# Kernel tuning notes

Hardware: AMD Instinct MI355X
Metric: run time of the kernel (lower is better)

Reference implementation:

```python
import jax, jax.numpy as jnp
import numpy as np

EPS = 1e-5


def setup_inputs() -> dict:
    key = jax.random.key(0)
    ks = jax.random.split(key, 6)
    B, N, F = 8, 8192, 64
    xyzs = jax.random.uniform(ks[0], (B, N, 3), dtype=jnp.float32)
    feats = jax.random.normal(ks[1], (B, N, F), dtype=jnp.float32)
    c_in = 3 + F  # 67
    dims = [(64, c_in), (64, 64), (128, 64)]
    inp = {"xyzs": xyzs, "feats": feats}
    for i, (co, ci) in enumerate(dims, start=1):
        inp[f"w{i}"] = jax.random.normal(ks[1 + i], (co, ci), dtype=jnp.float32) / np.sqrt(ci)
        inp[f"b{i}"] = jnp.zeros((co,), jnp.float32)
        inp[f"g{i}"] = jnp.ones((co,), jnp.float32)
        inp[f"bt{i}"] = jnp.zeros((co,), jnp.float32)
        inp[f"m{i}"] = jnp.zeros((co,), jnp.float32)
        inp[f"v{i}"] = jnp.ones((co,), jnp.float32)
    return inp


def sample_farthest_points(xyz, S):
    # Iterative FPS starting from index 0 (pytorch3d default random_start_point=False).
    B, N, _ = xyz.shape
    barange = jnp.arange(B)

    def step(carry, _):
        mind, last = carry                      # mind: [B,N] min sq-dist to selected set
        lastp = xyz[barange, last]              # [B,3]
        d = jnp.sum((xyz - lastp[:, None, :]) ** 2, -1)
        mind = jnp.minimum(mind, d)
        nxt = jnp.argmax(mind, axis=1).astype(jnp.int32)
        return (mind, nxt), nxt

    init = (jnp.full((B, N), 1e10, xyz.dtype), jnp.zeros((B,), jnp.int32))
    _, rest = jax.lax.scan(step, init, None, length=S - 1)  # [S-1, B]
    idx = jnp.concatenate([jnp.zeros((1, B), jnp.int32), rest], 0).T  # [B,S]
    return xyz[barange[:, None], idx], idx


def ball_query(centers, xyz, K, radius):
    # First-K-in-radius semantics of pytorch3d.ops.ball_query; pad idx with -1,
    # pad gathered points with zeros (masked_gather behavior).
    B, N, _ = xyz.shape
    d2 = (jnp.sum(centers ** 2, -1)[:, :, None]
          + jnp.sum(xyz ** 2, -1)[:, None, :]
          - 2.0 * jnp.einsum('bsd,bnd->bsn', centers, xyz))  # [B,S,N]
    within = d2 <= radius * radius
    skey = jnp.where(within, jnp.arange(N, dtype=jnp.int32), N)
    negvals, idx = jax.lax.top_k(-skey, K)      # K smallest keys = first K in-radius
    valid = (-negvals) < N                       # [B,S,K]
    group_idx = jnp.where(valid, idx, -1)
    gathered = xyz[jnp.arange(B)[:, None, None], jnp.where(valid, idx, 0)]  # [B,S,K,3]
    group_xyz = jnp.where(valid[..., None], gathered, 0.0)
    return group_idx, group_xyz


def _mlp_layer(x, w, b, g, bt, m, v):
    # 1x1 Conv2d over channel axis + BatchNorm (eval stats) + ReLU; x: [B,S,K,Cin]
    y = jnp.einsum('bskc,oc->bsko', x, w) + b
    y = g * (y - m) * jax.lax.rsqrt(v + EPS) + bt
    return jax.nn.relu(y)


def reference(xyzs, feats, w1, b1, g1, bt1, m1, v1,
              w2, b2, g2, bt2, m2, v2, w3, b3, g3, bt3, m3, v3):
    S, K, radius = 2048, 32, 0.2
    B = xyzs.shape[0]
    center_xyzs, _ = sample_farthest_points(xyzs, S)             # [B,S,3]
    group_idxs, group_xyzs = ball_query(center_xyzs, xyzs, K, radius)
    group_xyzs = group_xyzs - center_xyzs[:, :, None, :]          # relative coords
    batch_idxs = jnp.arange(B)[:, None, None]
    gf = feats[batch_idxs, jnp.where(group_idxs < 0, 0, group_idxs)]  # [B,S,K,F]
    gf = jnp.concatenate([group_xyzs, gf], axis=-1)
    gf = gf * (group_idxs != -1)[..., None].astype(gf.dtype)      # zero padded slots
    x = _mlp_layer(gf, w1, b1, g1, bt1, m1, v1)
    x = _mlp_layer(x, w2, b2, g2, bt2, m2, v2)
    x = _mlp_layer(x, w3, b3, g3, bt3, m3, v3)
    center_feats = jnp.max(x, axis=2)                             # max over neighbors
    return center_xyzs, center_feats
```

## Files before the change

kernel.cpp:

```cpp
#include <hip/hip_runtime.h>


#define NPTS 8192
#define SCTR 2048
#define NB   8
#define KNN  32
#define NF   64

typedef float v2f __attribute__((ext_vector_type(2)));

__device__ __forceinline__ v2f fps_sqdist_v2(v2f px, v2f py, v2f pz,
                                             v2f lx, v2f ly, v2f lz) {
#pragma clang fp contract(off)
  v2f dx = px - lx;
  v2f dy = py - ly;
  v2f dz = pz - lz;
  v2f xx = dx * dx;
  v2f yy = dy * dy;
  v2f zz = dz * dz;
  return (xx + yy) + zz;
}

__device__ __forceinline__ float sumsq3(float x, float y, float z) {
#pragma clang fp contract(off)
  return (x * x + y * y) + z * z;
}

__device__ __forceinline__ float bq_d2(float sc, float sx,
                                       float cx, float cy, float cz,
                                       float x, float y, float z) {
#pragma clang fp contract(off)
  float dt = fmaf(cz, z, fmaf(cy, y, cx * x));
  return (sc + sx) - 2.0f * dt;
}

template <int CTRL>
__device__ __forceinline__ unsigned long long kmax_dpp(unsigned long long k) {
  int lo = (int)(unsigned int)(k & 0xFFFFFFFFull);
  int hi = (int)(unsigned int)(k >> 32);
  int slo = __builtin_amdgcn_update_dpp(lo, lo, CTRL, 0xF, 0xF, false);
  int shi = __builtin_amdgcn_update_dpp(hi, hi, CTRL, 0xF, 0xF, false);
  unsigned long long sk =
      ((unsigned long long)(unsigned int)shi << 32) | (unsigned int)slo;
  return sk > k ? sk : k;
}

__global__ __launch_bounds__(256, 1) void fps_transpose_kernel(
    const float* __restrict__ xyzs,
    const float* __restrict__ w1, const float* __restrict__ w2, const float* __restrict__ w3,
    float* __restrict__ centers, float* __restrict__ wT)
{
  const int t = threadIdx.x;
  if (blockIdx.x >= NB) {
    int idx = (blockIdx.x - NB) * 256 + t;
    if (idx < 67*64) {
      int c = idx >> 6, o = idx & 63;
      wT[idx] = w1[o*67 + c];
    } else if (idx < 67*64 + 64*64) {
      int r = idx - 67*64; int c = r >> 6, o = r & 63;
      wT[idx] = w2[o*64 + c];
    } else if (idx < 67*64 + 64*64 + 64*128) {
      int r = idx - (67*64 + 64*64); int c = r >> 7, o = r & 127;
      wT[idx] = w3[o*64 + c];
    }
    return;
  }

  const int b = blockIdx.x;
  const float* xb = xyzs + (size_t)b * NPTS * 3;

  __shared__ float sX[NPTS], sY[NPTS], sZ[NPTS];
  __shared__ unsigned long long redk[2][4];
  __shared__ int hist[SCTR];

  for (int i = t; i < NPTS; i += 256) {
    sX[i] = xb[3*i+0];
    sY[i] = xb[3*i+1];
    sZ[i] = xb[3*i+2];
  }
  if (t == 0) hist[0] = 0;
  __syncthreads();

  const int t4 = 4 * t;

  const float4 xA = *(const float4*)(sX + 0    + t4);
  const float4 yA = *(const float4*)(sY + 0    + t4);
  const float4 zA = *(const float4*)(sZ + 0    + t4);
  const float4 xB = *(const float4*)(sX + 1024 + t4);
  const float4 yB = *(const float4*)(sY + 1024 + t4);
  const float4 zB = *(const float4*)(sZ + 1024 + t4);
  const float4 xC = *(const float4*)(sX + 2048 + t4);
  const float4 yC = *(const float4*)(sY + 2048 + t4);
  const float4 zC = *(const float4*)(sZ + 2048 + t4);
  const float4 xD = *(const float4*)(sX + 3072 + t4);
  const float4 yD = *(const float4*)(sY + 3072 + t4);
  const float4 zD = *(const float4*)(sZ + 3072 + t4);
  const float4 xE = *(const float4*)(sX + 4096 + t4);
  const float4 yE = *(const float4*)(sY + 4096 + t4);
  const float4 zE = *(const float4*)(sZ + 4096 + t4);
  const float4 xF = *(const float4*)(sX + 5120 + t4);
  const float4 yF = *(const float4*)(sY + 5120 + t4);
  const float4 zF = *(const float4*)(sZ + 5120 + t4);
  const float4 xG = *(const float4*)(sX + 6144 + t4);
  const float4 yG = *(const float4*)(sY + 6144 + t4);
  const float4 zG = *(const float4*)(sZ + 6144 + t4);
  const float4 xH = *(const float4*)(sX + 7168 + t4);
  const float4 yH = *(const float4*)(sY + 7168 + t4);
  const float4 zH = *(const float4*)(sZ + 7168 + t4);

  float4 mA = make_float4(1e10f,1e10f,1e10f,1e10f);
  float4 mB = mA, mC = mA, mD = mA, mE = mA, mF = mA, mG = mA, mH = mA;

  float lx = sX[0], ly = sY[0], lz = sZ[0];

#define FPS_QUAD(QX, QY, QZ, MV, QOFF, BV, BG)                                  \
  do {                                                                          \
    v2f d;                                                                      \
    d = fps_sqdist_v2((v2f){QX.x,QX.y}, (v2f){QY.x,QY.y}, (v2f){QZ.x,QZ.y},     \
                      lxv, lyv, lzv);                                           \
    MV.x = fminf(MV.x, d.x); if (MV.x > BV) { BV = MV.x; BG = (QOFF)+t4+0; }    \
    MV.y = fminf(MV.y, d.y); if (MV.y > BV) { BV = MV.y; BG = (QOFF)+t4+1; }    \
    d = fps_sqdist_v2((v2f){QX.z,QX.w}, (v2f){QY.z,QY.w}, (v2f){QZ.z,QZ.w},     \
                      lxv, lyv, lzv);                                           \
    MV.z = fminf(MV.z, d.x); if (MV.z > BV) { BV = MV.z; BG = (QOFF)+t4+2; }    \
    MV.w = fminf(MV.w, d.y); if (MV.w > BV) { BV = MV.w; BG = (QOFF)+t4+3; }    \
  } while (0)

  for (int s = 1; s < SCTR; ++s) {
    float bv0 = -1.0f, bv1 = -1.0f; int bg0 = 0, bg1 = 0;
    {
      v2f lxv = {lx, lx}, lyv = {ly, ly}, lzv = {lz, lz};
      FPS_QUAD(xA, yA, zA, mA, 0,    bv0, bg0);
      FPS_QUAD(xB, yB, zB, mB, 1024, bv0, bg0);
      FPS_QUAD(xC, yC, zC, mC, 2048, bv0, bg0);
      FPS_QUAD(xD, yD, zD, mD, 3072, bv0, bg0);
      FPS_QUAD(xE, yE, zE, mE, 4096, bv1, bg1);
      FPS_QUAD(xF, yF, zF, mF, 5120, bv1, bg1);
      FPS_QUAD(xG, yG, zG, mG, 6144, bv1, bg1);
      FPS_QUAD(xH, yH, zH, mH, 7168, bv1, bg1);
    }
    float bv = bv0; int bg = bg0;
    if (bv1 > bv0) { bv = bv1; bg = bg1; }

    unsigned long long key =
        ((unsigned long long)__float_as_uint(bv) << 13) |
        (unsigned long long)(8191 - bg);

    key = kmax_dpp<0x111>(key);
    key = kmax_dpp<0x112>(key);
    key = kmax_dpp<0x114>(key);
    key = kmax_dpp<0x118>(key);
    key = kmax_dpp<0x142>(key);
    key = kmax_dpp<0x143>(key);

    int pb = s & 1;
    if ((t & 63) == 63) redk[pb][t >> 6] = key;
    __syncthreads();

    unsigned long long k4 = redk[pb][t & 3];
    k4 = kmax_dpp<0xB1>(k4);
    k4 = kmax_dpp<0x4E>(k4);

    int i0 = 8191 - (int)(k4 & 0x1FFFull);
    lx = sX[i0]; ly = sY[i0]; lz = sZ[i0];
    if (t == 0) hist[s] = i0;
  }
#undef FPS_QUAD
  __syncthreads();

  for (int s = t; s < SCTR; s += 256) {
    int i = hist[s];
    float* o = centers + ((size_t)b * SCTR + s) * 3;
    o[0] = sX[i]; o[1] = sY[i]; o[2] = sZ[i];
  }
}

__global__ __launch_bounds__(128) void sa_fused_kernel(
    const float* __restrict__ xyzs, const float* __restrict__ feats,
    const float* centers, const float* __restrict__ wT,
    const float* __restrict__ b1, const float* __restrict__ g1, const float* __restrict__ bt1,
    const float* __restrict__ m1, const float* __restrict__ v1,
    const float* __restrict__ b2, const float* __restrict__ g2, const float* __restrict__ bt2,
    const float* __restrict__ m2, const float* __restrict__ v2,
    const float* __restrict__ b3, const float* __restrict__ g3, const float* __restrict__ bt3,
    const float* __restrict__ m3, const float* __restrict__ v3,
    float* out_feats)
{
  constexpr float R2 = (float)(0.2 * 0.2);
  const int bid  = blockIdx.x;
  const int b    = bid >> 11;
  const int tid  = threadIdx.x;
  const int w    = tid >> 6;
  const int lane = tid & 63;
  const float* xb = xyzs + (size_t)b * NPTS * 3;
  const float* cp = centers + (size_t)bid * 3;
  float cx = cp[0], cy = cp[1], cz = cp[2];
  float sc = sumsq3(cx, cy, cz);

  __shared__ int   gidx[KNN];
  __shared__ float in_[32*68];
  __shared__ float y_[32*68];

  int cnt = 0;
  for (int base = 0; base < NPTS && cnt < KNN; base += 64) {
    int n = base + lane;
    float x = xb[n*3+0], y = xb[n*3+1], z = xb[n*3+2];
    float sx = sumsq3(x, y, z);
    float d2 = bq_d2(sc, sx, cx, cy, cz, x, y, z);
    bool within = (d2 <= R2);
    unsigned long long mk = __ballot(within);
    int rank = __popcll(mk & ((1ull << lane) - 1ull));
    int slot = cnt + rank;
    if (within && slot < KNN) gidx[slot] = n;
    cnt += (int)__popcll(mk);
  }
  if (cnt > KNN) cnt = KNN;
  __syncthreads();

#pragma unroll 4
  for (int k2 = 0; k2 < 16; ++k2) {
    int k = 2*k2 + w;
    int gk = (k < cnt) ? gidx[k] : -1;
    float fv = 0.f, xv = 0.f;
    if (gk >= 0) {
      fv = feats[((size_t)b * NPTS + gk) * NF + lane];
      if (lane < 3) xv = xb[gk*3 + lane] - cp[lane];
    }
    in_[k*68 + 3 + lane] = fv;
    if (lane < 3) in_[k*68 + lane] = xv;
    if (lane == 3) in_[k*68 + 67] = 0.f;
  }
  __syncthreads();

  const int g  = lane >> 3;
  const int h  = lane & 7;
  const int ob = w*32 + 4*h;
  const float* w1T = wT;
  const float* w2T = wT + 67*64;
  const float* w3T = wT + 67*64 + 64*64;

#define FMA_COL(AS0, AS1, AS2, AS3, WV)                                      \
  do {                                                                       \
    acc[0][0]=fmaf(AS0, WV.x, acc[0][0]); acc[0][1]=fmaf(AS0, WV.y, acc[0][1]); \
    acc[0][2]=fmaf(AS0, WV.z, acc[0][2]); acc[0][3]=fmaf(AS0, WV.w, acc[0][3]); \
    acc[1][0]=fmaf(AS1, WV.x, acc[1][0]); acc[1][1]=fmaf(AS1, WV.y, acc[1][1]); \
    acc[1][2]=fmaf(AS1, WV.z, acc[1][2]); acc[1][3]=fmaf(AS1, WV.w, acc[1][3]); \
    acc[2][0]=fmaf(AS2, WV.x, acc[2][0]); acc[2][1]=fmaf(AS2, WV.y, acc[2][1]); \
    acc[2][2]=fmaf(AS2, WV.z, acc[2][2]); acc[2][3]=fmaf(AS2, WV.w, acc[2][3]); \
    acc[3][0]=fmaf(AS3, WV.x, acc[3][0]); acc[3][1]=fmaf(AS3, WV.y, acc[3][1]); \
    acc[3][2]=fmaf(AS3, WV.z, acc[3][2]); acc[3][3]=fmaf(AS3, WV.w, acc[3][3]); \
  } while (0)

#define MLP_CHUNK(SRC, WBASE, WSTRIDE, WOFF)                                 \
  do {                                                                       \
    float4 a0 = *(const float4*)(SRC + (4*g+0)*68 + c0);                     \
    float4 a1 = *(const float4*)(SRC + (4*g+1)*68 + c0);                     \
    float4 a2 = *(const float4*)(SRC + (4*g+2)*68 + c0);                     \
    float4 a3 = *(const float4*)(SRC + (4*g+3)*68 + c0);                     \
    float4 wv0 = *(const float4*)(WBASE + (c0+0)*(WSTRIDE) + (WOFF));        \
    float4 wv1 = *(const float4*)(WBASE + (c0+1)*(WSTRIDE) + (WOFF));        \
    float4 wv2 = *(const float4*)(WBASE + (c0+2)*(WSTRIDE) + (WOFF));        \
    float4 wv3 = *(const float4*)(WBASE + (c0+3)*(WSTRIDE) + (WOFF));        \
    FMA_COL(a0.x, a1.x, a2.x, a3.x, wv0);                                    \
    FMA_COL(a0.y, a1.y, a2.y, a3.y, wv1);                                    \
    FMA_COL(a0.z, a1.z, a2.z, a3.z, wv2);                                    \
    FMA_COL(a0.w, a1.w, a2.w, a3.w, wv3);                                    \
  } while (0)

  {
    float acc[4][4];
#pragma unroll
    for (int i=0;i<4;++i)
#pragma unroll
      for (int j=0;j<4;++j) acc[i][j]=0.f;
#pragma unroll 2
    for (int c0 = 0; c0 < 68; c0 += 4) {
      MLP_CHUNK(in_, w1T, 64, ob);
    }
    float scl[4], shf[4];
#pragma unroll
    for (int j=0;j<4;++j) {
      int o = ob + j;
      float r = g1[o] * rsqrtf(v1[o] + 1e-5f);
      scl[j] = r;
      shf[j] = (b1[o] - m1[o]) * r + bt1[o];
    }
#pragma unroll
    for (int i=0;i<4;++i) {
      float4 out;
      out.x = fmaxf(fmaf(acc[i][0], scl[0], shf[0]), 0.f);
      out.y = fmaxf(fmaf(acc[i][1], scl[1], shf[1]), 0.f);
      out.z = fmaxf(fmaf(acc[i][2], scl[2], shf[2]), 0.f);
      out.w = fmaxf(fmaf(acc[i][3], scl[3], shf[3]), 0.f);
      *(float4*)(y_ + (4*g+i)*68 + ob) = out;
    }
  }
  __syncthreads();

  {
    float acc[4][4];
#pragma unroll
    for (int i=0;i<4;++i)
#pragma unroll
      for (int j=0;j<4;++j) acc[i][j]=0.f;
#pragma unroll 2
    for (int c0 = 0; c0 < 64; c0 += 4) {
      MLP_CHUNK(y_, w2T, 64, ob);
    }
    float scl[4], shf[4];
#pragma unroll
    for (int j=0;j<4;++j) {
      int o = ob + j;
      float r = g2[o] * rsqrtf(v2[o] + 1e-5f);
      scl[j] = r;
      shf[j] = (b2[o] - m2[o]) * r + bt2[o];
    }
    __syncthreads();
#pragma unroll
    for (int i=0;i<4;++i) {
      float4 out;
      out.x = fmaxf(fmaf(acc[i][0], scl[0], shf[0]), 0.f);
      out.y = fmaxf(fmaf(acc[i][1], scl[1], shf[1]), 0.f);
      out.z = fmaxf(fmaf(acc[i][2], scl[2], shf[2]), 0.f);
      out.w = fmaxf(fmaf(acc[i][3], scl[3], shf[3]), 0.f);
      *(float4*)(in_ + (4*g+i)*68 + ob) = out;
    }
  }
  __syncthreads();

  for (int p = 0; p < 2; ++p) {
    const int o3 = w*64 + p*32 + 4*h;
    float acc[4][4];
#pragma unroll
    for (int i=0;i<4;++i)
#pragma unroll
      for (int j=0;j<4;++j) acc[i][j]=0.f;
#pragma unroll 2
    for (int c0 = 0; c0 < 64; c0 += 4) {
      MLP_CHUNK(in_, w3T, 128, o3);
    }
    float scl[4], shf[4];
#pragma unroll
    for (int j=0;j<4;++j) {
      int o = o3 + j;
      float r = g3[o] * rsqrtf(v3[o] + 1e-5f);
      scl[j] = r;
      shf[j] = (b3[o] - m3[o]) * r + bt3[o];
    }
    float vm[4];
#pragma unroll
    for (int j=0;j<4;++j) {
      float q0 = fmaxf(fmaf(acc[0][j], scl[j], shf[j]), 0.f);
      float q1 = fmaxf(fmaf(acc[1][j], scl[j], shf[j]), 0.f);
      float q2 = fmaxf(fmaf(acc[2][j], scl[j], shf[j]), 0.f);
      float q3 = fmaxf(fmaf(acc[3][j], scl[j], shf[j]), 0.f);
      vm[j] = fmaxf(fmaxf(q0,q1), fmaxf(q2,q3));
    }
#pragma unroll
    for (int mk = 8; mk < 64; mk <<= 1) {
#pragma unroll
      for (int j=0;j<4;++j) vm[j] = fmaxf(vm[j], __shfl_xor(vm[j], mk));
    }
    if (g == 0) {
      float* dst = out_feats + (size_t)bid*128 + o3;
      *(float4*)dst = make_float4(vm[0], vm[1], vm[2], vm[3]);
    }
  }
#undef MLP_CHUNK
#undef FMA_COL
}

extern "C" void kernel_launch(void* const* d_in, const int* in_sizes, int n_in,
                              void* d_out, int out_size, void* d_ws, size_t ws_size,
                              hipStream_t stream) {
  const float* xyzs  = (const float*)d_in[0];
  const float* feats = (const float*)d_in[1];
  const float* w1  = (const float*)d_in[2];
  const float* b1  = (const float*)d_in[3];
  const float* g1  = (const float*)d_in[4];
  const float* bt1 = (const float*)d_in[5];
  const float* m1  = (const float*)d_in[6];
  const float* v1  = (const float*)d_in[7];
  const float* w2  = (const float*)d_in[8];
  const float* b2  = (const float*)d_in[9];
  const float* g2  = (const float*)d_in[10];
  const float* bt2 = (const float*)d_in[11];
  const float* m2  = (const float*)d_in[12];
  const float* v2  = (const float*)d_in[13];
  const float* w3  = (const float*)d_in[14];
  const float* b3  = (const float*)d_in[15];
  const float* g3  = (const float*)d_in[16];
  const float* bt3 = (const float*)d_in[17];
  const float* m3  = (const float*)d_in[18];
  const float* v3  = (const float*)d_in[19];

  float* out       = (float*)d_out;
  float* centers   = out;
  float* out_feats = out + (size_t)NB * SCTR * 3;
  float* wT        = (float*)d_ws;

  hipLaunchKernelGGL(fps_transpose_kernel, dim3(NB + 65), dim3(256), 0, stream,
                     xyzs, w1, w2, w3, centers, wT);
  hipLaunchKernelGGL(sa_fused_kernel, dim3(NB * SCTR), dim3(128), 0, stream,
                     xyzs, feats, centers, wT,
                     b1, g1, bt1, m1, v1,
                     b2, g2, bt2, m2, v2,
                     b3, g3, bt3, m3, v3,
                     out_feats);
}
```

Before: 2.296 ms.

## Overlap FPS with grouping/MLP via persistent mega-kernel and progress flags

```diff
diff --git a/kernel.cpp b/kernel.cpp
--- a/kernel.cpp
+++ b/kernel.cpp
@@ -6,6 +6,8 @@
 #define NB   8
 #define KNN  32
 #define NF   64
+#define WT_FLOATS (67*64 + 64*64 + 64*128)
+#define PROG_STRIDE 32
 
 typedef float v2f __attribute__((ext_vector_type(2)));
 
@@ -45,73 +47,94 @@
   return sk > k ? sk : k;
 }
 
-__global__ __launch_bounds__(256, 1) void fps_transpose_kernel(
-    const float* __restrict__ xyzs,
-    const float* __restrict__ w1, const float* __restrict__ w2, const float* __restrict__ w3,
-    float* __restrict__ centers, float* __restrict__ wT)
+template <int CTRL>
+__device__ __forceinline__ void kmax_dpp_pay(unsigned long long& k,
+                                             float& x, float& y, float& z) {
+  int lo = (int)(unsigned int)(k & 0xFFFFFFFFull);
+  int hi = (int)(unsigned int)(k >> 32);
+  int slo = __builtin_amdgcn_update_dpp(lo, lo, CTRL, 0xF, 0xF, false);
+  int shi = __builtin_amdgcn_update_dpp(hi, hi, CTRL, 0xF, 0xF, false);
+  int sx  = __builtin_amdgcn_update_dpp(__float_as_int(x), __float_as_int(x), CTRL, 0xF, 0xF, false);
+  int sy  = __builtin_amdgcn_update_dpp(__float_as_int(y), __float_as_int(y), CTRL, 0xF, 0xF, false);
+  int sz  = __builtin_amdgcn_update_dpp(__float_as_int(z), __float_as_int(z), CTRL, 0xF, 0xF, false);
+  unsigned long long sk =
+      ((unsigned long long)(unsigned int)shi << 32) | (unsigned int)slo;
+  if (sk > k) {
+    k = sk;
+    x = __int_as_float(sx);
+    y = __int_as_float(sy);
+    z = __int_as_float(sz);
+  }
+}
+
+__global__ __launch_bounds__(256) void init_kernel(
+    const float* __restrict__ w1, const float* __restrict__ w2,
+    const float* __restrict__ w3, float* __restrict__ wT,
+    int* __restrict__ prog)
 {
   const int t = threadIdx.x;
-  if (blockIdx.x >= NB) {
-    int idx = (blockIdx.x - NB) * 256 + t;
-    if (idx < 67*64) {
-      int c = idx >> 6, o = idx & 63;
-      wT[idx] = w1[o*67 + c];
-    } else if (idx < 67*64 + 64*64) {
-      int r = idx - 67*64; int c = r >> 6, o = r & 63;
-      wT[idx] = w2[o*64 + c];
-    } else if (idx < 67*64 + 64*64 + 64*128) {
-      int r = idx - (67*64 + 64*64); int c = r >> 7, o = r & 127;
-      wT[idx] = w3[o*64 + c];
-    }
-    return;
-  }
-
-  const int b = blockIdx.x;
-  const float* xb = xyzs + (size_t)b * NPTS * 3;
-
-  __shared__ float sX[NPTS], sY[NPTS], sZ[NPTS];
-  __shared__ unsigned long long redk[2][4];
-  __shared__ int hist[SCTR];
-
-  for (int i = t; i < NPTS; i += 256) {
-    sX[i] = xb[3*i+0];
-    sY[i] = xb[3*i+1];
-    sZ[i] = xb[3*i+2];
-  }
-  if (t == 0) hist[0] = 0;
-  __syncthreads();
-
-  const int t4 = 4 * t;
-
-  const float4 xA = *(const float4*)(sX + 0    + t4);
-  const float4 yA = *(const float4*)(sY + 0    + t4);
-  const float4 zA = *(const float4*)(sZ + 0    + t4);
-  const float4 xB = *(const float4*)(sX + 1024 + t4);
-  const float4 yB = *(const float4*)(sY + 1024 + t4);
-  const float4 zB = *(const float4*)(sZ + 1024 + t4);
-  const float4 xC = *(const float4*)(sX + 2048 + t4);
-  const float4 yC = *(const float4*)(sY + 2048 + t4);
-  const float4 zC = *(const float4*)(sZ + 2048 + t4);
-  const float4 xD = *(const float4*)(sX + 3072 + t4);
-  const float4 yD = *(const float4*)(sY + 3072 + t4);
-  const float4 zD = *(const float4*)(sZ + 3072 + t4);
-  const float4 xE = *(const float4*)(sX + 4096 + t4);
-  const float4 yE = *(const float4*)(sY + 4096 + t4);
-  const float4 zE = *(const float4*)(sZ + 4096 + t4);
-  const float4 xF = *(const float4*)(sX + 5120 + t4);
-  const float4 yF = *(const float4*)(sY + 5120 + t4);
-  const float4 zF = *(const float4*)(sZ + 5120 + t4);
-  const float4 xG = *(const float4*)(sX + 6144 + t4);
-  const float4 yG = *(const float4*)(sY + 6144 + t4);
-  const float4 zG = *(const float4*)(sZ + 6144 + t4);
-  const float4 xH = *(const float4*)(sX + 7168 + t4);
-  const float4 yH = *(const float4*)(sY + 7168 + t4);
-  const float4 zH = *(const float4*)(sZ + 7168 + t4);
-
-  float4 mA = make_float4(1e10f,1e10f,1e10f,1e10f);
-  float4 mB = mA, mC = mA, mD = mA, mE = mA, mF = mA, mG = mA, mH = mA;
-
-  float lx = sX[0], ly = sY[0], lz = sZ[0];
+  if (blockIdx.x == 0 && t < NB) prog[t * PROG_STRIDE] = 0;
+  int idx = blockIdx.x * 256 + t;
+  if (idx < 67*64) {
+    int c = idx >> 6, o = idx & 63;
+    wT[idx] = w1[o*67 + c];
+  } else if (idx < 67*64 + 64*64) {
+    int r = idx - 67*64; int c = r >> 6, o = r & 63;
+    wT[idx] = w2[o*64 + c];
+  } else if (idx < 67*64 + 64*64 + 64*128) {
+    int r = idx - (67*64 + 64*64); int c = r >> 7, o = r & 127;
+    wT[idx] = w3[o*64 + c];
+  }
+}
+
+__global__ __launch_bounds__(256, 1) void mega_kernel(
+    const float* __restrict__ xyzs, const float* __restrict__ feats,
+    float* centers, const float* __restrict__ wT, int* prog,
+    const float* __restrict__ b1, const float* __restrict__ g1, const float* __restrict__ bt1,
+    const float* __restrict__ m1, const float* __restrict__ v1,
+    const float* __restrict__ b2, const float* __restrict__ g2, const float* __restrict__ bt2,
+    const float* __restrict__ m2, const float* __restrict__ v2,
+    const float* __restrict__ b3, const float* __restrict__ g3, const float* __restrict__ bt3,
+    const float* __restrict__ m3, const float* __restrict__ v3,
+    float* out_feats)
+{
+  __shared__ __align__(16) float smem[8784];
+
+  if (blockIdx.x < NB) {
+    __builtin_amdgcn_s_setprio(3);
+    const int b = blockIdx.x;
+    const int t = threadIdx.x;
+    const int t4 = 4 * t;
+    const float* xb = xyzs + (size_t)b * NPTS * 3;
+    int* prog_b = prog + b * PROG_STRIDE;
+    float* cb_ = centers + (size_t)b * SCTR * 3;
+
+#define LOADQ(QX, QY, QZ, QOFF)                                               \
+    { const float4* p_ = (const float4*)(xb + (size_t)3 * ((QOFF) + t4));     \
+      float4 l0 = p_[0], l1 = p_[1], l2 = p_[2];                              \
+      QX = make_float4(l0.x, l0.w, l1.z, l2.y);                               \
+      QY = make_float4(l0.y, l1.x, l1.w, l2.z);                               \
+      QZ = make_float4(l0.z, l1.y, l2.x, l2.w); }
+
+    float4 xA, yA, zA, xB, yB, zB, xC, yC, zC, xD, yD, zD;
+    float4 xE, yE, zE, xF, yF, zF, xG, yG, zG, xH, yH, zH;
+    LOADQ(xA, yA, zA, 0);
+    LOADQ(xB, yB, zB, 1024);
+    LOADQ(xC, yC, zC, 2048);
+    LOADQ(xD, yD, zD, 3072);
+    LOADQ(xE, yE, zE, 4096);
+    LOADQ(xF, yF, zF, 5120);
+    LOADQ(xG, yG, zG, 6144);
+    LOADQ(xH, yH, zH, 7168);
+#undef LOADQ
+
+    float4 mA = make_float4(1e10f, 1e10f, 1e10f, 1e10f);
+    float4 mB = mA, mC = mA, mD = mA, mE = mA, mF = mA, mG = mA, mH = mA;
+
+    if (t == 0) { smem[0] = xA.x; smem[1] = yA.x; smem[2] = zA.x; }
+    __syncthreads();
+    float lx = smem[0], ly = smem[1], lz = smem[2];
+    if (t == 0) { cb_[0] = lx; cb_[1] = ly; cb_[2] = lz; }
 
 #define FPS_QUAD(QX, QY, QZ, MV, QOFF, BV, BG)                                  \
   do {                                                                          \
@@ -126,80 +149,118 @@
     MV.w = fminf(MV.w, d.y); if (MV.w > BV) { BV = MV.w; BG = (QOFF)+t4+3; }    \
   } while (0)
 
-  for (int s = 1; s < SCTR; ++s) {
-    float bv0 = -1.0f, bv1 = -1.0f; int bg0 = 0, bg1 = 0;
-    {
-      v2f lxv = {lx, lx}, lyv = {ly, ly}, lzv = {lz, lz};
-      FPS_QUAD(xA, yA, zA, mA, 0,    bv0, bg0);
-      FPS_QUAD(xB, yB, zB, mB, 1024, bv0, bg0);
-      FPS_QUAD(xC, yC, zC, mC, 2048, bv0, bg0);
-      FPS_QUAD(xD, yD, zD, mD, 3072, bv0, bg0);
-      FPS_QUAD(xE, yE, zE, mE, 4096, bv1, bg1);
-      FPS_QUAD(xF, yF, zF, mF, 5120, bv1, bg1);
-      FPS_QUAD(xG, yG, zG, mG, 6144, bv1, bg1);
-      FPS_QUAD(xH, yH, zH, mH, 7168, bv1, bg1);
-    }
-    float bv = bv0; int bg = bg0;
-    if (bv1 > bv0) { bv = bv1; bg = bg1; }
-
-    unsigned long long key =
-        ((unsigned long long)__float_as_uint(bv) << 13) |
-        (unsigned long long)(8191 - bg);
-
-    key = kmax_dpp<0x111>(key);
-    key = kmax_dpp<0x112>(key);
-    key = kmax_dpp<0x114>(key);
-    key = kmax_dpp<0x118>(key);
-    key = kmax_dpp<0x142>(key);
-    key = kmax_dpp<0x143>(key);
-
-    int pb = s & 1;
-    if ((t & 63) == 63) redk[pb][t >> 6] = key;
-    __syncthreads();
-
-    unsigned long long k4 = redk[pb][t & 3];
-    k4 = kmax_dpp<0xB1>(k4);
-    k4 = kmax_dpp<0x4E>(k4);
-
-    int i0 = 8191 - (int)(k4 & 0x1FFFull);
-    lx = sX[i0]; ly = sY[i0]; lz = sZ[i0];
-    if (t == 0) hist[s] = i0;
-  }
+    for (int s = 1; s < SCTR; ++s) {
+      float bv0 = -1.0f, bv1 = -1.0f; int bg0 = 0, bg1 = 0;
+      {
+        v2f lxv = {lx, lx}, lyv = {ly, ly}, lzv = {lz, lz};
+        FPS_QUAD(xA, yA, zA, mA, 0,    bv0, bg0);
+        FPS_QUAD(xB, yB, zB, mB, 1024, bv0, bg0);
+        FPS_QUAD(xC, yC, zC, mC, 2048, bv0, bg0);
+        FPS_QUAD(xD, yD, zD, mD, 3072, bv0, bg0);
+        FPS_QUAD(xE, yE, zE, mE, 4096, bv1, bg1);
+        FPS_QUAD(xF, yF, zF, mF, 5120, bv1, bg1);
+        FPS_QUAD(xG, yG, zG, mG, 6144, bv1, bg1);
+        FPS_QUAD(xH, yH, zH, mH, 7168, bv1, bg1);
+      }
+      float bv = bv0; int bg = bg0;
+      if (bv1 > bv0) { bv = bv1; bg = bg1; }
+
+      unsigned long long key =
+          ((unsigned long long)__float_as_uint(bv) << 13) |
+          (unsigned long long)(8191 - bg);
+
+      key = kmax_dpp<0x111>(key);
+      key = kmax_dpp<0x112>(key);
+      key = kmax_dpp<0x114>(key);
+      key = kmax_dpp<0x118>(key);
+      key = kmax_dpp<0x142>(key);
+      key = kmax_dpp<0x143>(key);
+      int skl = __builtin_amdgcn_readlane((int)(unsigned int)(key & 0xFFFFFFFFull), 63);
+      int skh = __builtin_amdgcn_readlane((int)(unsigned int)(key >> 32), 63);
+      int widx = 8191 - (skl & 0x1FFF);
+      int q = widx >> 10;
+      int j = widx & 3;
+      int othr = (widx & 1023) >> 2;
+      float wx = 0.f, wy = 0.f, wz = 0.f;
+      if (t == othr) {
+        float4 qx, qy, qz;
+        switch (q) {
+          case 0: qx = xA; qy = yA; qz = zA; break;
+          case 1: qx = xB; qy = yB; qz = zB; break;
+          case 2: qx = xC; qy = yC; qz = zC; break;
+          case 3: qx = xD; qy = yD; qz = zD; break;
+          case 4: qx = xE; qy = yE; qz = zE; break;
+          case 5: qx = xF; qy = yF; qz = zF; break;
+          case 6: qx = xG; qy = yG; qz = zG; break;
+          default: qx = xH; qy = yH; qz = zH; break;
+        }
+        wx = (j == 0) ? qx.x : ((j == 1) ? qx.y : ((j == 2) ? qx.z : qx.w));
+        wy = (j == 0) ? qy.x : ((j == 1) ? qy.y : ((j == 2) ? qy.z : qy.w));
+        wz = (j == 0) ? qz.x : ((j == 1) ? qz.y : ((j == 2) ? qz.z : qz.w));
+      }
+      int ol = othr & 63;
+      wx = __int_as_float(__builtin_amdgcn_readlane(__float_as_int(wx), ol));
+      wy = __int_as_float(__builtin_amdgcn_readlane(__float_as_int(wy), ol));
+      wz = __int_as_float(__builtin_amdgcn_readlane(__float_as_int(wz), ol));
+
+      int pb = s & 1;
+      if ((t & 63) == 63) {
+        float* slot = smem + (size_t)((pb * 4 + (t >> 6)) * 8);
+        slot[0] = __int_as_float(skl);
+        slot[1] = __int_as_float(skh);
+        slot[2] = wx; slot[3] = wy; slot[4] = wz;
+      }
+      __syncthreads();
+      const float* rs = smem + (size_t)((pb * 4 + (t & 3)) * 8);
+      unsigned long long k4 =
+          ((unsigned long long)(unsigned int)__float_as_int(rs[1]) << 32) |
+          (unsigned int)__float_as_int(rs[0]);
+      float px = rs[2], py = rs[3], pz = rs[4];
+      kmax_dpp_pay<0xB1>(k4, px, py, pz);
+      kmax_dpp_pay<0x4E>(k4, px, py, pz);
+      lx = px; ly = py; lz = pz;
+
+      if (t == 0) {
+        float* o = cb_ + 3 * s;
+        o[0] = lx; o[1] = ly; o[2] = lz;
+        if ((s & 31) == 31)
+          __hip_atomic_store(prog_b, s + 1, __ATOMIC_RELEASE, __HIP_MEMORY_SCOPE_AGENT);
+      }
+    }
 #undef FPS_QUAD
+    return;
+  }
+
+  constexpr float R2 = (float)(0.2 * 0.2);
+  const int t    = threadIdx.x;
+  const int jb   = blockIdx.x - NB;
+  const int half = t >> 7;
+  const int ht   = t & 127;
+  const int w    = ht >> 6;
+  const int lane = ht & 63;
+  const int cid  = 2 * jb + half;
+  const int b    = cid & 7;
+  const int s    = cid >> 3;
+  const int bid  = b * SCTR + s;
+  const float* xb = xyzs + (size_t)b * NPTS * 3;
+
+  float* in_  = smem + half * 4352;
+  float* y_   = in_ + 2176;
+  int*   gidx = (int*)(smem + 8704) + half * KNN;
+  float* csl  = smem + 8768 + half * 4;
+
+  if (ht == 0) {
+    int* pb_ = prog + b * PROG_STRIDE;
+    while (__hip_atomic_load(pb_, __ATOMIC_RELAXED, __HIP_MEMORY_SCOPE_AGENT) <= s)
+      __builtin_amdgcn_s_sleep(64);
+    const int* cg = (const int*)(centers + (size_t)bid * 3);
+    csl[0] = __int_as_float(__hip_atomic_load(cg + 0, __ATOMIC_RELAXED, __HIP_MEMORY_SCOPE_AGENT));
+    csl[1] = __int_as_float(__hip_atomic_load(cg + 1, __ATOMIC_RELAXED, __HIP_MEMORY_SCOPE_AGENT));
+    csl[2] = __int_as_float(__hip_atomic_load(cg + 2, __ATOMIC_RELAXED, __HIP_MEMORY_SCOPE_AGENT));
+  }
   __syncthreads();
-
-  for (int s = t; s < SCTR; s += 256) {
-    int i = hist[s];
-    float* o = centers + ((size_t)b * SCTR + s) * 3;
-    o[0] = sX[i]; o[1] = sY[i]; o[2] = sZ[i];
-  }
-}
-
-__global__ __launch_bounds__(128) void sa_fused_kernel(
-    const float* __restrict__ xyzs, const float* __restrict__ feats,
-    const float* centers, const float* __restrict__ wT,
-    const float* __restrict__ b1, const float* __restrict__ g1, const float* __restrict__ bt1,
-    const float* __restrict__ m1, const float* __restrict__ v1,
-    const float* __restrict__ b2, const float* __restrict__ g2, const float* __restrict__ bt2,
-    const float* __restrict__ m2, const float* __restrict__ v2,
-    const float* __restrict__ b3, const float* __restrict__ g3, const float* __restrict__ bt3,
-    const float* __restrict__ m3, const float* __restrict__ v3,
-    float* out_feats)
-{
-  constexpr float R2 = (float)(0.2 * 0.2);
-  const int bid  = blockIdx.x;
-  const int b    = bid >> 11;
-  const int tid  = threadIdx.x;
-  const int w    = tid >> 6;
-  const int lane = tid & 63;
-  const float* xb = xyzs + (size_t)b * NPTS * 3;
-  const float* cp = centers + (size_t)bid * 3;
-  float cx = cp[0], cy = cp[1], cz = cp[2];
-  float sc = sumsq3(cx, cy, cz);
-
-  __shared__ int   gidx[KNN];
-  __shared__ float in_[32*68];
-  __shared__ float y_[32*68];
+  const float cx = csl[0], cy = csl[1], cz = csl[2];
+  const float sc = sumsq3(cx, cy, cz);
 
   int cnt = 0;
   for (int base = 0; base < NPTS && cnt < KNN; base += 64) {
@@ -224,7 +285,7 @@
     float fv = 0.f, xv = 0.f;
     if (gk >= 0) {
       fv = feats[((size_t)b * NPTS + gk) * NF + lane];
-      if (lane < 3) xv = xb[gk*3 + lane] - cp[lane];
+      if (lane < 3) xv = xb[gk*3 + lane] - csl[lane];
     }
     in_[k*68 + 3 + lane] = fv;
     if (lane < 3) in_[k*68 + lane] = xv;
@@ -253,10 +314,10 @@
 
 #define MLP_CHUNK(SRC, WBASE, WSTRIDE, WOFF)                                 \
   do {                                                                       \
-    float4 a0 = *(const float4*)(SRC + (4*g+0)*68 + c0);                     \
-    float4 a1 = *(const float4*)(SRC + (4*g+1)*68 + c0);                     \
-    float4 a2 = *(const float4*)(SRC + (4*g+2)*68 + c0);                     \
-    float4 a3 = *(const float4*)(SRC + (4*g+3)*68 + c0);                     \
+    float4 a0 = *(const float4*)((SRC) + (4*g+0)*68 + c0);                   \
+    float4 a1 = *(const float4*)((SRC) + (4*g+1)*68 + c0);                   \
+    float4 a2 = *(const float4*)((SRC) + (4*g+2)*68 + c0);                   \
+    float4 a3 = *(const float4*)((SRC) + (4*g+3)*68 + c0);                   \
     float4 wv0 = *(const float4*)(WBASE + (c0+0)*(WSTRIDE) + (WOFF));        \
     float4 wv1 = *(const float4*)(WBASE + (c0+1)*(WSTRIDE) + (WOFF));        \
     float4 wv2 = *(const float4*)(WBASE + (c0+2)*(WSTRIDE) + (WOFF));        \
@@ -398,11 +459,12 @@
   float* centers   = out;
   float* out_feats = out + (size_t)NB * SCTR * 3;
   float* wT        = (float*)d_ws;
-
-  hipLaunchKernelGGL(fps_transpose_kernel, dim3(NB + 65), dim3(256), 0, stream,
-                     xyzs, w1, w2, w3, centers, wT);
-  hipLaunchKernelGGL(sa_fused_kernel, dim3(NB * SCTR), dim3(128), 0, stream,
-                     xyzs, feats, centers, wT,
+  int*   prog      = (int*)((float*)d_ws + WT_FLOATS);
+
+  hipLaunchKernelGGL(init_kernel, dim3(65), dim3(256), 0, stream,
+                     w1, w2, w3, wT, prog);
+  hipLaunchKernelGGL(mega_kernel, dim3(NB + NB * SCTR / 2), dim3(256), 0, stream,
+                     xyzs, feats, centers, wT, prog,
                      b1, g1, bt1, m1, v1,
                      b2, g2, bt2, m2, v2,
                      b3, g3, bt3, m3, v3,
```

After: 2.386 ms. 1.04x slower.

## Overlap FPS with grouping/MLP via persistent mega-kernel and progress flags

Applied to the files above, without the earlier changes.

```diff
diff --git a/kernel.cpp b/kernel.cpp
--- a/kernel.cpp
+++ b/kernel.cpp
@@ -6,6 +6,8 @@
 #define NB   8
 #define KNN  32
 #define NF   64
+#define WT_FLOATS (67*64 + 64*64 + 64*128)
+#define PROG_STRIDE 32
 
 typedef float v2f __attribute__((ext_vector_type(2)));
 
@@ -45,73 +47,92 @@
   return sk > k ? sk : k;
 }
 
-__global__ __launch_bounds__(256, 1) void fps_transpose_kernel(
-    const float* __restrict__ xyzs,
-    const float* __restrict__ w1, const float* __restrict__ w2, const float* __restrict__ w3,
-    float* __restrict__ centers, float* __restrict__ wT)
+__global__ __launch_bounds__(256) void init_kernel(
+    const float* __restrict__ w1, const float* __restrict__ w2,
+    const float* __restrict__ w3, float* __restrict__ wT,
+    int* __restrict__ prog)
 {
   const int t = threadIdx.x;
-  if (blockIdx.x >= NB) {
-    int idx = (blockIdx.x - NB) * 256 + t;
-    if (idx < 67*64) {
-      int c = idx >> 6, o = idx & 63;
-      wT[idx] = w1[o*67 + c];
-    } else if (idx < 67*64 + 64*64) {
-      int r = idx - 67*64; int c = r >> 6, o = r & 63;
-      wT[idx] = w2[o*64 + c];
-    } else if (idx < 67*64 + 64*64 + 64*128) {
-      int r = idx - (67*64 + 64*64); int c = r >> 7, o = r & 127;
-      wT[idx] = w3[o*64 + c];
-    }
-    return;
-  }
-
-  const int b = blockIdx.x;
-  const float* xb = xyzs + (size_t)b * NPTS * 3;
-
-  __shared__ float sX[NPTS], sY[NPTS], sZ[NPTS];
-  __shared__ unsigned long long redk[2][4];
-  __shared__ int hist[SCTR];
-
-  for (int i = t; i < NPTS; i += 256) {
-    sX[i] = xb[3*i+0];
-    sY[i] = xb[3*i+1];
-    sZ[i] = xb[3*i+2];
-  }
-  if (t == 0) hist[0] = 0;
-  __syncthreads();
-
-  const int t4 = 4 * t;
-
-  const float4 xA = *(const float4*)(sX + 0    + t4);
-  const float4 yA = *(const float4*)(sY + 0    + t4);
-  const float4 zA = *(const float4*)(sZ + 0    + t4);
-  const float4 xB = *(const float4*)(sX + 1024 + t4);
-  const float4 yB = *(const float4*)(sY + 1024 + t4);
-  const float4 zB = *(const float4*)(sZ + 1024 + t4);
-  const float4 xC = *(const float4*)(sX + 2048 + t4);
-  const float4 yC = *(const float4*)(sY + 2048 + t4);
-  const float4 zC = *(const float4*)(sZ + 2048 + t4);
-  const float4 xD = *(const float4*)(sX + 3072 + t4);
-  const float4 yD = *(const float4*)(sY + 3072 + t4);
-  const float4 zD = *(const float4*)(sZ + 3072 + t4);
-  const float4 xE = *(const float4*)(sX + 4096 + t4);
-  const float4 yE = *(const float4*)(sY + 4096 + t4);
-  const float4 zE = *(const float4*)(sZ + 4096 + t4);
-  const float4 xF = *(const float4*)(sX + 5120 + t4);
-  const float4 yF = *(const float4*)(sY + 5120 + t4);
-  const float4 zF = *(const float4*)(sZ + 5120 + t4);
-  const float4 xG = *(const float4*)(sX + 6144 + t4);
-  const float4 yG = *(const float4*)(sY + 6144 + t4);
-  const float4 zG = *(const float4*)(sZ + 6144 + t4);
-  const float4 xH = *(const float4*)(sX + 7168 + t4);
-  const float4 yH = *(const float4*)(sY + 7168 + t4);
-  const float4 zH = *(const float4*)(sZ + 7168 + t4);
-
-  float4 mA = make_float4(1e10f,1e10f,1e10f,1e10f);
-  float4 mB = mA, mC = mA, mD = mA, mE = mA, mF = mA, mG = mA, mH = mA;
-
-  float lx = sX[0], ly = sY[0], lz = sZ[0];
+  if (blockIdx.x == 0) prog[t] = 0;
+  int idx = blockIdx.x * 256 + t;
+  if (idx < 67*64) {
+    int c = idx >> 6, o = idx & 63;
+    wT[idx] = w1[o*67 + c];
+  } else if (idx < 67*64 + 64*64) {
+    int r = idx - 67*64; int c = r >> 6, o = r & 63;
+    wT[idx] = w2[o*64 + c];
+  } else if (idx < 67*64 + 64*64 + 64*128) {
+    int r = idx - (67*64 + 64*64); int c = r >> 7, o = r & 127;
+    wT[idx] = w3[o*64 + c];
+  }
+}
+
+__global__ __launch_bounds__(256, 1) void mega_kernel(
+    const float* __restrict__ xyzs, const float* __restrict__ feats,
+    float* centers, const float* __restrict__ wT, int* prog,
+    const float* __restrict__ b1, const float* __restrict__ g1, const float* __restrict__ bt1,
+    const float* __restrict__ m1, const float* __restrict__ v1,
+    const float* __restrict__ b2, const float* __restrict__ g2, const float* __restrict__ bt2,
+    const float* __restrict__ m2, const float* __restrict__ v2,
+    const float* __restrict__ b3, const float* __restrict__ g3, const float* __restrict__ bt3,
+    const float* __restrict__ m3, const float* __restrict__ v3,
+    float* out_feats)
+{
+  __shared__ __align__(16) float smem[26640];
+
+  if (blockIdx.x < NB) {
+    __builtin_amdgcn_s_setprio(3);
+    const int b = blockIdx.x;
+    const int t = threadIdx.x;
+    const float* xb = xyzs + (size_t)b * NPTS * 3;
+    int* prog_b = prog + b * PROG_STRIDE;
+    float* cb_ = centers + (size_t)b * SCTR * 3;
+
+    float* sX = smem;
+    float* sY = smem + 8192;
+    float* sZ = smem + 16384;
+    int*  hist = (int*)(smem + 24576);
+    unsigned long long* redk = (unsigned long long*)(smem + 26624);
+
+    for (int i = t; i < NPTS; i += 256) {
+      sX[i] = xb[3*i+0];
+      sY[i] = xb[3*i+1];
+      sZ[i] = xb[3*i+2];
+    }
+    if (t == 0) hist[0] = 0;
+    __syncthreads();
+
+    const int t4 = 4 * t;
+
+    const float4 xA = *(const float4*)(sX + 0    + t4);
+    const float4 yA = *(const float4*)(sY + 0    + t4);
+    const float4 zA = *(const float4*)(sZ + 0    + t4);
+    const float4 xB = *(const float4*)(sX + 1024 + t4);
+    const float4 yB = *(const float4*)(sY + 1024 + t4);
+    const float4 zB = *(const float4*)(sZ + 1024 + t4);
+    const float4 xC = *(const float4*)(sX + 2048 + t4);
+    const float4 yC = *(const float4*)(sY + 2048 + t4);
+    const float4 zC = *(const float4*)(sZ + 2048 + t4);
+    const float4 xD = *(const float4*)(sX + 3072 + t4);
+    const float4 yD = *(const float4*)(sY + 3072 + t4);
+    const float4 zD = *(const float4*)(sZ + 3072 + t4);
+    const float4 xE = *(const float4*)(sX + 4096 + t4);
+    const float4 yE = *(const float4*)(sY + 4096 + t4);
+    const float4 zE = *(const float4*)(sZ + 4096 + t4);
+    const float4 xF = *(const float4*)(sX + 5120 + t4);
+    const float4 yF = *(const float4*)(sY + 5120 + t4);
+    const float4 zF = *(const float4*)(sZ + 5120 + t4);
+    const float4 xG = *(const float4*)(sX + 6144 + t4);
+    const float4 yG = *(const float4*)(sY + 6144 + t4);
+    const float4 zG = *(const float4*)(sZ + 6144 + t4);
+    const float4 xH = *(const float4*)(sX + 7168 + t4);
+    const float4 yH = *(const float4*)(sY + 7168 + t4);
+    const float4 zH = *(const float4*)(sZ + 7168 + t4);
+
+    float4 mA = make_float4(1e10f,1e10f,1e10f,1e10f);
+    float4 mB = mA, mC = mA, mD = mA, mE = mA, mF = mA, mG = mA, mH = mA;
+
+    float lx = sX[0], ly = sY[0], lz = sZ[0];
 
 #define FPS_QUAD(QX, QY, QZ, MV, QOFF, BV, BG)                                  \
   do {                                                                          \
@@ -126,80 +147,92 @@
     MV.w = fminf(MV.w, d.y); if (MV.w > BV) { BV = MV.w; BG = (QOFF)+t4+3; }    \
   } while (0)
 
-  for (int s = 1; s < SCTR; ++s) {
-    float bv0 = -1.0f, bv1 = -1.0f; int bg0 = 0, bg1 = 0;
-    {
-      v2f lxv = {lx, lx}, lyv = {ly, ly}, lzv = {lz, lz};
-      FPS_QUAD(xA, yA, zA, mA, 0,    bv0, bg0);
-      FPS_QUAD(xB, yB, zB, mB, 1024, bv0, bg0);
-      FPS_QUAD(xC, yC, zC, mC, 2048, bv0, bg0);
-      FPS_QUAD(xD, yD, zD, mD, 3072, bv0, bg0);
-      FPS_QUAD(xE, yE, zE, mE, 4096, bv1, bg1);
-      FPS_QUAD(xF, yF, zF, mF, 5120, bv1, bg1);
-      FPS_QUAD(xG, yG, zG, mG, 6144, bv1, bg1);
-      FPS_QUAD(xH, yH, zH, mH, 7168, bv1, bg1);
-    }
-    float bv = bv0; int bg = bg0;
-    if (bv1 > bv0) { bv = bv1; bg = bg1; }
-
-    unsigned long long key =
-        ((unsigned long long)__float_as_uint(bv) << 13) |
-        (unsigned long long)(8191 - bg);
-
-    key = kmax_dpp<0x111>(key);
-    key = kmax_dpp<0x112>(key);
-    key = kmax_dpp<0x114>(key);
-    key = kmax_dpp<0x118>(key);
-    key = kmax_dpp<0x142>(key);
-    key = kmax_dpp<0x143>(key);
-
-    int pb = s & 1;
-    if ((t & 63) == 63) redk[pb][t >> 6] = key;
-    __syncthreads();
-
-    unsigned long long k4 = redk[pb][t & 3];
-    k4 = kmax_dpp<0xB1>(k4);
-    k4 = kmax_dpp<0x4E>(k4);
-
-    int i0 = 8191 - (int)(k4 & 0x1FFFull);
-    lx = sX[i0]; ly = sY[i0]; lz = sZ[i0];
-    if (t == 0) hist[s] = i0;
-  }
+    for (int s = 1; s < SCTR; ++s) {
+      float bv0 = -1.0f, bv1 = -1.0f; int bg0 = 0, bg1 = 0;
+      {
+        v2f lxv = {lx, lx}, lyv = {ly, ly}, lzv = {lz, lz};
+        FPS_QUAD(xA, yA, zA, mA, 0,    bv0, bg0);
+        FPS_QUAD(xB, yB, zB, mB, 1024, bv0, bg0);
+        FPS_QUAD(xC, yC, zC, mC, 2048, bv0, bg0);
+        FPS_QUAD(xD, yD, zD, mD, 3072, bv0, bg0);
+        FPS_QUAD(xE, yE, zE, mE, 4096, bv1, bg1);
+        FPS_QUAD(xF, yF, zF, mF, 5120, bv1, bg1);
+        FPS_QUAD(xG, yG, zG, mG, 6144, bv1, bg1);
+        FPS_QUAD(xH, yH, zH, mH, 7168, bv1, bg1);
+      }
+      float bv = bv0; int bg = bg0;
+      if (bv1 > bv0) { bv = bv1; bg = bg1; }
+
+      unsigned long long key =
+          ((unsigned long long)__float_as_uint(bv) << 13) |
+          (unsigned long long)(8191 - bg);
+
+      key = kmax_dpp<0x111>(key);
+      key = kmax_dpp<0x112>(key);
+      key = kmax_dpp<0x114>(key);
+      key = kmax_dpp<0x118>(key);
+      key = kmax_dpp<0x142>(key);
+      key = kmax_dpp<0x143>(key);
+
+      int pb = s & 1;
+      if ((t & 63) == 63) redk[pb*4 + (t >> 6)] = key;
+      __syncthreads();
+
+      unsigned long long k4 = redk[pb*4 + (t & 3)];
+      k4 = kmax_dpp<0xB1>(k4);
+      k4 = kmax_dpp<0x4E>(k4);
+
+      int i0 = 8191 - (int)(k4 & 0x1FFFull);
+      lx = sX[i0]; ly = sY[i0]; lz = sZ[i0];
+      if (t == 0) hist[s] = i0;
+
+      if ((s & 31) == 31) {
+        if (t < 32) {
+          int ci  = (s - 31) + t;
+          int idx = hist[ci];
+          float x = sX[idx], y = sY[idx], z = sZ[idx];
+          float* o = cb_ + 3*ci;
+          o[0] = x; o[1] = y; o[2] = z;
+        }
+        if (t == 0)
+          __hip_atomic_store(prog_b, s - 31, __ATOMIC_RELEASE, __HIP_MEMORY_SCOPE_AGENT);
+      }
+    }
 #undef FPS_QUAD
+    __builtin_amdgcn_s_sleep(127);
+    if (t == 0)
+      __hip_atomic_store(prog_b, SCTR, __ATOMIC_RELEASE, __HIP_MEMORY_SCOPE_AGENT);
+    return;
+  }
+
+  constexpr float R2 = (float)(0.2 * 0.2);
+  const int t    = threadIdx.x;
+  const int jb   = blockIdx.x - NB;
+  const int half = t >> 7;
+  const int ht   = t & 127;
+  const int w    = ht >> 6;
+  const int lane = ht & 63;
+  const int cid  = 2 * jb + half;
+  const int b    = cid & 7;
+  const int s    = cid >> 3;
+  const int bid  = b * SCTR + s;
+  const float* xb = xyzs + (size_t)b * NPTS * 3;
+
+  float* in_  = smem + half * 4352;
+  float* y_   = in_ + 2176;
+  int*   gidx = (int*)(smem + 8704) + half * KNN;
+  float* csl  = smem + 8768 + half * 4;
+
+  if (ht == 0) {
+    int* pb_ = prog + b * PROG_STRIDE;
+    while (__hip_atomic_load(pb_, __ATOMIC_ACQUIRE, __HIP_MEMORY_SCOPE_AGENT) <= s)
+      __builtin_amdgcn_s_sleep(64);
+    const float* cg = centers + (size_t)bid * 3;
+    csl[0] = cg[0]; csl[1] = cg[1]; csl[2] = cg[2];
+  }
   __syncthreads();
-
-  for (int s = t; s < SCTR; s += 256) {
-    int i = hist[s];
-    float* o = centers + ((size_t)b * SCTR + s) * 3;
-    o[0] = sX[i]; o[1] = sY[i]; o[2] = sZ[i];
-  }
-}
-
-__global__ __launch_bounds__(128) void sa_fused_kernel(
-    const float* __restrict__ xyzs, const float* __restrict__ feats,
-    const float* centers, const float* __restrict__ wT,
-    const float* __restrict__ b1, const float* __restrict__ g1, const float* __restrict__ bt1,
-    const float* __restrict__ m1, const float* __restrict__ v1,
-    const float* __restrict__ b2, const float* __restrict__ g2, const float* __restrict__ bt2,
-    const float* __restrict__ m2, const float* __restrict__ v2,
-    const float* __restrict__ b3, const float* __restrict__ g3, const float* __restrict__ bt3,
-    const float* __restrict__ m3, const float* __restrict__ v3,
-    float* out_feats)
-{
-  constexpr float R2 = (float)(0.2 * 0.2);
-  const int bid  = blockIdx.x;
-  const int b    = bid >> 11;
-  const int tid  = threadIdx.x;
-  const int w    = tid >> 6;
-  const int lane = tid & 63;
-  const float* xb = xyzs + (size_t)b * NPTS * 3;
-  const float* cp = centers + (size_t)bid * 3;
-  float cx = cp[0], cy = cp[1], cz = cp[2];
-  float sc = sumsq3(cx, cy, cz);
-
-  __shared__ int   gidx[KNN];
-  __shared__ float in_[32*68];
-  __shared__ float y_[32*68];
+  const float cx = csl[0], cy = csl[1], cz = csl[2];
+  const float sc = sumsq3(cx, cy, cz);
 
   int cnt = 0;
   for (int base = 0; base < NPTS && cnt < KNN; base += 64) {
@@ -224,7 +257,7 @@
     float fv = 0.f, xv = 0.f;
     if (gk >= 0) {
       fv = feats[((size_t)b * NPTS + gk) * NF + lane];
-      if (lane < 3) xv = xb[gk*3 + lane] - cp[lane];
+      if (lane < 3) xv = xb[gk*3 + lane] - csl[lane];
     }
     in_[k*68 + 3 + lane] = fv;
     if (lane < 3) in_[k*68 + lane] = xv;
@@ -253,10 +286,10 @@
 
 #define MLP_CHUNK(SRC, WBASE, WSTRIDE, WOFF)                                 \
   do {                                                                       \
-    float4 a0 = *(const float4*)(SRC + (4*g+0)*68 + c0);                     \
-    float4 a1 = *(const float4*)(SRC + (4*g+1)*68 + c0);                     \
-    float4 a2 = *(const float4*)(SRC + (4*g+2)*68 + c0);                     \
-    float4 a3 = *(const float4*)(SRC + (4*g+3)*68 + c0);                     \
+    float4 a0 = *(const float4*)((SRC) + (4*g+0)*68 + c0);                   \
+    float4 a1 = *(const float4*)((SRC) + (4*g+1)*68 + c0);                   \
+    float4 a2 = *(const float4*)((SRC) + (4*g+2)*68 + c0);                   \
+    float4 a3 = *(const float4*)((SRC) + (4*g+3)*68 + c0);                   \
     float4 wv0 = *(const float4*)(WBASE + (c0+0)*(WSTRIDE) + (WOFF));        \
     float4 wv1 = *(const float4*)(WBASE + (c0+1)*(WSTRIDE) + (WOFF));        \
     float4 wv2 = *(const float4*)(WBASE + (c0+2)*(WSTRIDE) + (WOFF));        \
@@ -398,11 +431,12 @@
   float* centers   = out;
   float* out_feats = out + (size_t)NB * SCTR * 3;
   float* wT        = (float*)d_ws;
-
-  hipLaunchKernelGGL(fps_transpose_kernel, dim3(NB + 65), dim3(256), 0, stream,
-                     xyzs, w1, w2, w3, centers, wT);
-  hipLaunchKernelGGL(sa_fused_kernel, dim3(NB * SCTR), dim3(128), 0, stream,
-                     xyzs, feats, centers, wT,
+  int*   prog      = (int*)((float*)d_ws + WT_FLOATS);
+
+  hipLaunchKernelGGL(init_kernel, dim3(65), dim3(256), 0, stream,
+                     w1, w2, w3, wT, prog);
+  hipLaunchKernelGGL(mega_kernel, dim3(NB + NB * SCTR / 2), dim3(256), 0, stream,
+                     xyzs, feats, centers, wT, prog,
                      b1, g1, bt1, m1, v1,
                      b2, g2, bt2, m2, v2,
                      b3, g3, bt3, m3, v3,
```

After: 2.030 ms. 11.6% less time.
